# Optimization experiments

Measured on AMD Instinct MI355X. Metric: run time of the kernel, lower is better.

The kernel has to match this reference:

```python
import jax, jax.numpy as jnp
import numpy as np

B, L, E, R, A = 1024, 40, 1024, 1024, 512


def setup_inputs() -> dict:
    key = jax.random.key(0)
    ks = jax.random.split(key, 20)
    s = 0.05  # weight scale to avoid gate saturation
    inp = {
        "xt": jax.random.normal(ks[0], (B, E), jnp.float32),
        "xt_mask": jnp.ones((B, 1), jnp.float32),
        "V": jax.random.normal(ks[1], (B, L, R), jnp.float32),
        "pos_feat": jax.random.normal(ks[2], (B, R), jnp.float32),
        "h1": jax.random.normal(ks[3], (1, B, R), jnp.float32),
        "c1": jax.random.normal(ks[4], (1, B, R), jnp.float32),
        "h2": jax.random.normal(ks[5], (1, B, R), jnp.float32),
        "c2": jax.random.normal(ks[6], (1, B, R), jnp.float32),
        "Wg": jax.random.normal(ks[7], (E, R), jnp.float32) * s,
        "bg": jnp.zeros((R,), jnp.float32),
        "Wi1": jax.random.normal(ks[8], (E, 4 * R), jnp.float32) * s,
        "bi1": jnp.zeros((4 * R,), jnp.float32),
        "Wa1": jax.random.normal(ks[9], (R, 4 * R), jnp.float32) * s,
        "ba1": jnp.zeros((4 * R,), jnp.float32),
        "Wh1": jax.random.normal(ks[10], (R, 4 * R), jnp.float32) * s,
        "bh1": jnp.zeros((4 * R,), jnp.float32),
        "Wi2": jax.random.normal(ks[11], (R, 4 * R), jnp.float32) * s,
        "bi2": jnp.zeros((4 * R,), jnp.float32),
        "Wa2": jax.random.normal(ks[12], (R, 4 * R), jnp.float32) * s,
        "ba2": jnp.zeros((4 * R,), jnp.float32),
        "Wh2": jax.random.normal(ks[13], (R, 4 * R), jnp.float32) * s,
        "bh2": jnp.zeros((4 * R,), jnp.float32),
        "Wv2a": jax.random.normal(ks[14], (R, A), jnp.float32) * s,
        "bv2a": jnp.zeros((A,), jnp.float32),
        "Wh2a": jax.random.normal(ks[15], (2 * R, A), jnp.float32) * s,
        "bh2a": jnp.zeros((A,), jnp.float32),
        "Wa2w": jax.random.normal(ks[16], (A, 1), jnp.float32) * s,
        "ba2w": jnp.zeros((1,), jnp.float32),
    }
    return inp


def _lstm_cell(in1, in2, h, c, Wi, bi, Wa, ba, Wh, bh, mask):
    # all_input_sums: [B, 4R]; torch gate order: i, f, o (sigmoid) then g (tanh)
    s = in1 @ Wi + bi + in2 @ Wa + ba + h @ Wh + bh
    i_g = jax.nn.sigmoid(s[:, 0 * R:1 * R])
    f_g = jax.nn.sigmoid(s[:, 1 * R:2 * R])
    o_g = jax.nn.sigmoid(s[:, 2 * R:3 * R])
    g = jnp.tanh(s[:, 3 * R:4 * R])
    c_new = f_g * c + i_g * g
    c_new = c_new * mask + c * (1.0 - mask)
    h_new = o_g * jnp.tanh(c_new)
    h_new = h_new * mask + h * (1.0 - mask)
    return h_new, c_new


def reference(xt, xt_mask, V, pos_feat, h1, c1, h2, c2,
              Wg, bg, Wi1, bi1, Wa1, ba1, Wh1, bh1,
              Wi2, bi2, Wa2, ba2, Wh2, bh2,
              Wv2a, bv2a, Wh2a, bh2a, Wa2w, ba2w):
    h1l, c1l = h1[-1], c1[-1]  # [B, R]
    h2l, c2l = h2[-1], c2[-1]
    # additive attention over L frames
    hq = jnp.concatenate([h1l, h2l], axis=1) @ Wh2a + bh2a        # [B, A]
    e = jnp.tanh(hq[:, None, :] + V @ Wv2a + bv2a) @ Wa2w + ba2w  # [B, L, 1]
    w = jax.nn.softmax(e, axis=1)                                  # softmax over L
    af = jnp.sum(w * V, axis=1)                                    # [B, R]
    # gate (dropout in eval mode -> identity)
    gate = jax.nn.relu(xt @ Wg + bg)
    gated_pos = gate * pos_feat + pos_feat
    # two-layer LSTM
    out1, c1n = _lstm_cell(xt, gated_pos, h1l, c1l, Wi1, bi1, Wa1, ba1, Wh1, bh1, xt_mask)
    out2, c2n = _lstm_cell(out1, af, h2l, c2l, Wi2, bi2, Wa2, ba2, Wh2, bh2, xt_mask)
    return (out2, out1[None], c1n[None], out2[None], c2n[None])
```

## Files before the change

### kernel.cpp

```cpp
#include <hip/hip_runtime.h>
#include <math.h>

#define BB 1024
#define LL 40
#define RR 1024

using short8 = __attribute__((ext_vector_type(8))) short;
using us8    = __attribute__((ext_vector_type(8))) unsigned short;
using f32x4  = __attribute__((ext_vector_type(4))) float;

__device__ __forceinline__ ushort f2bf(float f) {
    union { float f; unsigned u; } a; a.f = f;
    unsigned r = a.u + 0x7fffu + ((a.u >> 16) & 1u);
    return (ushort)(r >> 16);
}
__device__ __forceinline__ float bf2f(ushort u) {
    union { unsigned u; float f; } a; a.u = ((unsigned)u) << 16;
    return a.f;
}
__device__ __forceinline__ float ftanh(float x) {
    float cx = fminf(fmaxf(x, -15.f), 15.f);
    float e = __expf(2.f * cx);
    return (e - 1.f) / (e + 1.f);
}
__device__ __forceinline__ float fsigmoid(float x) {
    float cx = fminf(fmaxf(x, -30.f), 30.f);
    return 1.f / (1.f + __expf(-cx));
}

__device__ __forceinline__ void gll16(const ushort* g, ushort* l) {
    __builtin_amdgcn_global_load_lds(
        (const __attribute__((address_space(1))) void*)g,
        (__attribute__((address_space(3))) void*)l,
        16, 0, 0);
}

__global__ __launch_bounds__(256) void conv_bf16_kernel(
    const float* __restrict__ src, ushort* __restrict__ dst, int n8)
{
    const int i = blockIdx.x * 256 + threadIdx.x;
    if (i >= n8) return;
    const float4* s4 = (const float4*)(src + (size_t)i * 8);
    float4 x = s4[0], y = s4[1];
    us8 v;
    v[0] = f2bf(x.x); v[1] = f2bf(x.y); v[2] = f2bf(x.z); v[3] = f2bf(x.w);
    v[4] = f2bf(y.x); v[5] = f2bf(y.y); v[6] = f2bf(y.z); v[7] = f2bf(y.w);
    ((us8*)dst)[i] = v;
}

struct CP3 { const float* in[3]; ushort* out[3]; };
__global__ __launch_bounds__(256) void conv_bf16_batch3_kernel(CP3 p, int n8)
{
    const int z = blockIdx.y;
    const int i = blockIdx.x * 256 + threadIdx.x;
    if (i >= n8) return;
    const float4* s4 = (const float4*)(p.in[z] + (size_t)i * 8);
    float4 x = s4[0], y = s4[1];
    us8 v;
    v[0] = f2bf(x.x); v[1] = f2bf(x.y); v[2] = f2bf(x.z); v[3] = f2bf(x.w);
    v[4] = f2bf(y.x); v[5] = f2bf(y.y); v[6] = f2bf(y.z); v[7] = f2bf(y.w);
    ((us8*)p.out[z])[i] = v;
}

struct TP6 { const float* in[6]; ushort* out[6]; int N[6]; };
__global__ __launch_bounds__(256) void transpose_conv_kernel(TP6 p)
{
    const int z = blockIdx.z;
    const int Nn = p.N[z];
    const int n0 = blockIdx.x * 64;
    if (n0 >= Nn) return;
    const int k0 = blockIdx.y * 64;
    const float* in = p.in[z];
    ushort* out = p.out[z];

    __shared__ float tile[64][65];
    const int t = threadIdx.x;
    const int tx = t & 63, ty = t >> 6;
#pragma unroll
    for (int r = 0; r < 16; ++r) {
        const int row = ty * 16 + r;
        tile[row][tx] = in[(size_t)(k0 + row) * Nn + n0 + tx];
    }
    __syncthreads();
    const int n = t >> 2, kq = t & 3;
    us8 v0, v1;
#pragma unroll
    for (int j = 0; j < 8; ++j) v0[j] = f2bf(tile[kq * 16 + j][n]);
#pragma unroll
    for (int j = 0; j < 8; ++j) v1[j] = f2bf(tile[kq * 16 + 8 + j][n]);
    ushort* op = out + (size_t)(n0 + n) * 1024 + k0 + kq * 16;
    *(us8*)op = v0;
    *((us8*)op + 1) = v1;
}

template <int NP, int SK>
__global__ __launch_bounds__(256) void gemm_gl(
    const ushort* __restrict__ A0, const ushort* __restrict__ A1, const ushort* __restrict__ A2,
    const ushort* __restrict__ W0, const ushort* __restrict__ W1, const ushort* __restrict__ W2,
    ushort* __restrict__ Cp, int M, int N)
{
    __shared__ ushort As[128 * 64];
    __shared__ ushort Bs[128 * 64];

    const int t = threadIdx.x, l = t & 63, w = t >> 6;
    const int wm = w >> 1, wn = w & 1;
    const int m0 = blockIdx.y * 128, n0 = blockIdx.x * 128;

    const int srow = l >> 3;
    const int csw  = ((l & 7) ^ (l >> 3)) * 8;
    const int kx0 = ((0 + (l >> 4)) ^ (l & 7)) * 8;
    const int kx1 = ((4 + (l >> 4)) ^ (l & 7)) * 8;

    f32x4 acc[4][4];
#pragma unroll
    for (int i = 0; i < 4; ++i)
#pragma unroll
        for (int j = 0; j < 4; ++j) acc[i][j] = (f32x4){0.f, 0.f, 0.f, 0.f};

    const int total = NP * 16;
    const int per   = total / SK;
    const int s0v   = blockIdx.z * per;
    const int sEnd  = s0v + per;

    for (int s = s0v; s < sEnd; ++s) {
        const int p  = (NP == 1) ? 0 : (s >> 4);
        const int k0 = (s & 15) << 6;
        const ushort* Ap = (p == 0) ? A0 : ((p == 1) ? A1 : A2);
        const ushort* Wp = (p == 0) ? W0 : ((p == 1) ? W1 : W2);
#pragma unroll
        for (int j = 0; j < 4; ++j) {
            const int rb = w * 32 + j * 8;
            gll16(Ap + (size_t)(m0 + rb + srow) * 1024 + k0 + csw, &As[rb * 64]);
            gll16(Wp + (size_t)(n0 + rb + srow) * 1024 + k0 + csw, &Bs[rb * 64]);
        }
        __syncthreads();

        short8 aF[4][2], bF[4][2];
#pragma unroll
        for (int mi = 0; mi < 4; ++mi) {
            const int ro = (wm * 64 + mi * 16 + (l & 15)) * 64;
            aF[mi][0] = *(const short8*)&As[ro + kx0];
            aF[mi][1] = *(const short8*)&As[ro + kx1];
        }
#pragma unroll
        for (int ni = 0; ni < 4; ++ni) {
            const int ro = (wn * 64 + ni * 16 + (l & 15)) * 64;
            bF[ni][0] = *(const short8*)&Bs[ro + kx0];
            bF[ni][1] = *(const short8*)&Bs[ro + kx1];
        }
#pragma unroll
        for (int mi = 0; mi < 4; ++mi)
#pragma unroll
            for (int ni = 0; ni < 4; ++ni) {
                acc[mi][ni] = __builtin_amdgcn_mfma_f32_16x16x32_bf16(
                    aF[mi][0], bF[ni][0], acc[mi][ni], 0, 0, 0);
                acc[mi][ni] = __builtin_amdgcn_mfma_f32_16x16x32_bf16(
                    aF[mi][1], bF[ni][1], acc[mi][ni], 0, 0, 0);
            }
        __syncthreads();
    }

    ushort* Cz = Cp + (size_t)blockIdx.z * M * N;
#pragma unroll
    for (int ni = 0; ni < 4; ++ni) {
        const int col = n0 + wn * 64 + ni * 16 + (l & 15);
#pragma unroll
        for (int mi = 0; mi < 4; ++mi) {
            const int row = m0 + wm * 64 + mi * 16 + ((l >> 4) << 2);
#pragma unroll
            for (int r = 0; r < 4; ++r)
                Cz[(size_t)(row + r) * N + col] = f2bf(acc[mi][ni][r]);
        }
    }
}

__global__ __launch_bounds__(256) void attn_db(
    const ushort* __restrict__ A0, const ushort* __restrict__ W0,
    const float* __restrict__ hq, const float* __restrict__ bv2a,
    const float* __restrict__ Wa2w, float* __restrict__ epart)
{
    __shared__ ushort As[2][128 * 32];
    __shared__ ushort Bs[2][128 * 32];

    const int t = threadIdx.x, l = t & 63, w = t >> 6;
    const int wm = w >> 1, wn = w & 1;

    const int lin = blockIdx.y * gridDim.x + blockIdx.x;
    const int swz = (lin & 7) * 160 + (lin >> 3);
    const int bx = swz & 3, by = swz >> 2;
    const int m0 = by * 128, n0 = bx * 128;

    const int srow  = l >> 2;
    const int schnk = ((l & 3) ^ ((l >> 3) & 3)) * 8;

    int aoff[4], boff[4];
#pragma unroll
    for (int mi = 0; mi < 4; ++mi)
        aoff[mi] = (wm * 64 + mi * 16 + (l & 15)) * 32 + (((l >> 4) ^ ((l >> 1) & 3)) * 8);
#pragma unroll
    for (int ni = 0; ni < 4; ++ni)
        boff[ni] = (wn * 64 + ni * 16 + (l & 15)) * 32 + (((l >> 4) ^ ((l >> 1) & 3)) * 8);

    f32x4 acc[4][4];
#pragma unroll
    for (int i = 0; i < 4; ++i)
#pragma unroll
        for (int j = 0; j < 4; ++j) acc[i][j] = (f32x4){0.f, 0.f, 0.f, 0.f};

    auto stage = [&](int s, int buf) {
        const int k0 = s << 5;
#pragma unroll
        for (int j = 0; j < 2; ++j) {
            const int rb = j * 64 + w * 16;
            gll16(A0 + (size_t)(m0 + rb + srow) * 1024 + k0 + schnk, &As[buf][rb * 32]);
            gll16(W0 + (size_t)(n0 + rb + srow) * 1024 + k0 + schnk, &Bs[buf][rb * 32]);
        }
    };

    constexpr int NS = 32;
    stage(0, 0);
    int cur = 0;
    for (int s = 0; s < NS; ++s) {
        const bool pf = (s + 1 < NS);
        if (pf) {
            stage(s + 1, cur ^ 1);
            asm volatile("s_waitcnt vmcnt(4)" ::: "memory");
        } else {
            asm volatile("s_waitcnt vmcnt(0)" ::: "memory");
        }
        __builtin_amdgcn_s_barrier();
        asm volatile("" ::: "memory");

        short8 aF[4], bF[4];
#pragma unroll
        for (int mi = 0; mi < 4; ++mi) aF[mi] = *(const short8*)&As[cur][aoff[mi]];
#pragma unroll
        for (int ni = 0; ni < 4; ++ni) bF[ni] = *(const short8*)&Bs[cur][boff[ni]];
#pragma unroll
        for (int mi = 0; mi < 4; ++mi)
#pragma unroll
            for (int ni = 0; ni < 4; ++ni)
                acc[mi][ni] = __builtin_amdgcn_mfma_f32_16x16x32_bf16(
                    aF[mi], bF[ni], acc[mi][ni], 0, 0, 0);

        asm volatile("" ::: "memory");
        __builtin_amdgcn_s_barrier();
        asm volatile("" ::: "memory");
        cur ^= 1;
    }

    float* red = (float*)&As[0][0];
    float wa[4], bv[4];
    int coln[4];
#pragma unroll
    for (int ni = 0; ni < 4; ++ni) {
        coln[ni] = n0 + wn * 64 + ni * 16 + (l & 15);
        wa[ni] = Wa2w[coln[ni]];
        bv[ni] = bv2a[coln[ni]];
    }
#pragma unroll
    for (int mi = 0; mi < 4; ++mi) {
        const int rowl = wm * 64 + mi * 16 + ((l >> 4) << 2);
#pragma unroll
        for (int r = 0; r < 4; ++r) {
            const int row = m0 + rowl + r;
            const int b = row / LL;
            float v = 0.f;
#pragma unroll
            for (int ni = 0; ni < 4; ++ni) {
                float x = acc[mi][ni][r] + hq[(size_t)b * 512 + coln[ni]] + bv[ni];
                v += ftanh(x) * wa[ni];
            }
            v += __shfl_xor(v, 1);
            v += __shfl_xor(v, 2);
            v += __shfl_xor(v, 4);
            v += __shfl_xor(v, 8);
            if ((l & 15) == 0) red[(rowl + r) * 2 + wn] = v;
        }
    }
    __syncthreads();
    if (t < 128)
        epart[(size_t)(m0 + t) * 4 + bx] = red[t * 2] + red[t * 2 + 1];
}

__global__ __launch_bounds__(256) void reduce_hq_b_kernel(
    const ushort* __restrict__ part, const float* __restrict__ bias, float* __restrict__ hq)
{
    const int i = blockIdx.x * 256 + threadIdx.x;
    float s = bias[i & 511];
#pragma unroll
    for (int z = 0; z < 8; ++z) s += bf2f(part[(size_t)z * 524288 + i]);
    hq[i] = s;
}

__global__ __launch_bounds__(256) void reduce_gate_b_kernel(
    const ushort* __restrict__ part, const float* __restrict__ bias,
    const float* __restrict__ pos, ushort* __restrict__ gpb)
{
    const int i = blockIdx.x * 256 + threadIdx.x;
    float s = bias[i & 1023];
#pragma unroll
    for (int z = 0; z < 4; ++z) s += bf2f(part[(size_t)z * 1048576 + i]);
    const float g = fmaxf(s, 0.f);
    gpb[i] = f2bf(g * pos[i] + pos[i]);
}

__global__ __launch_bounds__(256) void softmax_af_kernel(
    const float* __restrict__ epart, const ushort* __restrict__ Vb,
    const float* __restrict__ ba2w, ushort* __restrict__ afb)
{
    const int b = blockIdx.x;
    const int tid = threadIdx.x;
    __shared__ float e_raw[LL];
    __shared__ float e_exp[LL];

    if (tid < LL) {
        const float* ep = &epart[(size_t)(b * LL + tid) * 4];
        float e = ba2w[0];
#pragma unroll
        for (int c = 0; c < 4; ++c) e += ep[c];
        e_raw[tid] = e;
    }
    __syncthreads();
    float mx = -1e30f;
#pragma unroll
    for (int ll = 0; ll < LL; ++ll) mx = fmaxf(mx, e_raw[ll]);
    if (tid < LL) e_exp[tid] = __expf(e_raw[tid] - mx);
    __syncthreads();
    float sum = 0.f;
#pragma unroll
    for (int ll = 0; ll < LL; ++ll) sum += e_exp[ll];
    const float inv = 1.f / sum;

    const int r4 = tid * 4;
    const ushort* vp = &Vb[(size_t)b * LL * RR + r4];
    float a0 = 0.f, a1 = 0.f, a2 = 0.f, a3 = 0.f;
#pragma unroll 8
    for (int ll = 0; ll < LL; ++ll) {
        ushort4 v = *(const ushort4*)&vp[(size_t)ll * RR];
        const float wgt = e_exp[ll];
        a0 += wgt * bf2f(v.x); a1 += wgt * bf2f(v.y);
        a2 += wgt * bf2f(v.z); a3 += wgt * bf2f(v.w);
    }
    ushort* op = &afb[(size_t)b * RR + r4];
    op[0] = f2bf(a0 * inv); op[1] = f2bf(a1 * inv);
    op[2] = f2bf(a2 * inv); op[3] = f2bf(a3 * inv);
}

__global__ __launch_bounds__(256) void lstm_finishb_kernel(
    const ushort* __restrict__ part,
    const float* __restrict__ bi, const float* __restrict__ ba, const float* __restrict__ bh,
    const float* __restrict__ c_in, const float* __restrict__ h_in, const float* __restrict__ mask,
    float* __restrict__ h_out, float* __restrict__ h_out2,
    float* __restrict__ c_out, ushort* __restrict__ h_bf)
{
    const int i = blockIdx.x * 256 + threadIdx.x;
    const int b = i >> 10;
    const int r = i & 1023;
    float sg[4];
#pragma unroll
    for (int g = 0; g < 4; ++g) {
        const int gr = g * 1024 + r;
        float s = bi[gr] + ba[gr] + bh[gr];
#pragma unroll
        for (int z = 0; z < 4; ++z)
            s += bf2f(part[(size_t)z * 4194304 + (size_t)b * 4096 + gr]);
        sg[g] = s;
    }
    const float ig = fsigmoid(sg[0]);
    const float fg = fsigmoid(sg[1]);
    const float og = fsigmoid(sg[2]);
    const float gt = ftanh(sg[3]);
    const float m = mask[b];
    const float c = c_in[i];
    float cn = fg * c + ig * gt;
    cn = cn * m + c * (1.f - m);
    const float h = h_in[i];
    float hn = og * ftanh(cn);
    hn = hn * m + h * (1.f - m);
    h_out[i] = hn;
    if (h_out2) h_out2[i] = hn;
    c_out[i] = cn;
    if (h_bf) h_bf[i] = f2bf(hn);
}

extern "C" void kernel_launch(void* const* d_in, const int* in_sizes, int n_in,
                              void* d_out, int out_size, void* d_ws, size_t ws_size,
                              hipStream_t stream) {
    const float* xt   = (const float*)d_in[0];
    const float* mask = (const float*)d_in[1];
    const float* V    = (const float*)d_in[2];
    const float* pos  = (const float*)d_in[3];
    const float* h1   = (const float*)d_in[4];
    const float* c1   = (const float*)d_in[5];
    const float* h2   = (const float*)d_in[6];
    const float* c2   = (const float*)d_in[7];
    const float* Wg   = (const float*)d_in[8];
    const float* bg   = (const float*)d_in[9];
    const float* Wi1  = (const float*)d_in[10];
    const float* bi1  = (const float*)d_in[11];
    const float* Wa1  = (const float*)d_in[12];
    const float* ba1  = (const float*)d_in[13];
    const float* Wh1  = (const float*)d_in[14];
    const float* bh1  = (const float*)d_in[15];
    const float* Wi2  = (const float*)d_in[16];
    const float* bi2  = (const float*)d_in[17];
    const float* Wa2  = (const float*)d_in[18];
    const float* ba2  = (const float*)d_in[19];
    const float* Wh2  = (const float*)d_in[20];
    const float* bh2  = (const float*)d_in[21];
    const float* Wv2a = (const float*)d_in[22];
    const float* bv2a = (const float*)d_in[23];
    const float* Wh2a = (const float*)d_in[24];
    const float* bh2a = (const float*)d_in[25];
    const float* Wa2w = (const float*)d_in[26];
    const float* ba2w = (const float*)d_in[27];

    float* out = (float*)d_out;
    float* out2  = out;
    float* out1  = out + (size_t)BB * RR;
    float* c1n   = out + 2 * (size_t)BB * RR;
    float* out2b = out + 3 * (size_t)BB * RR;
    float* c2n   = out + 4 * (size_t)BB * RR;

    ushort* wsu = (ushort*)d_ws;
    size_t o = 0;
    ushort* Vb     = wsu + o; o += (size_t)40960 * 1024;
    ushort* Wh2aT0 = wsu + o; o += (size_t)512 * 1024;
    ushort* Wh2aT1 = wsu + o; o += (size_t)512 * 1024;
    ushort* WgT    = wsu + o; o += (size_t)1024 * 1024;
    ushort* Wv2aT  = wsu + o; o += (size_t)512 * 1024;
    ushort* Wi1T   = wsu + o; o += (size_t)4096 * 1024;
    ushort* Wa1T   = wsu + o; o += (size_t)4096 * 1024;
    ushort* Wh1T   = wsu + o; o += (size_t)4096 * 1024;
    ushort* Wi2T   = wsu + o; o += (size_t)4096 * 1024;
    ushort* Wa2T   = wsu + o; o += (size_t)4096 * 1024;
    ushort* Wh2T   = wsu + o; o += (size_t)4096 * 1024;
    ushort* xtb    = wsu + o; o += (size_t)1024 * 1024;
    ushort* h1b    = wsu + o; o += (size_t)1024 * 1024;
    ushort* h2b    = wsu + o; o += (size_t)1024 * 1024;
    ushort* gpb    = wsu + o; o += (size_t)1024 * 1024;
    ushort* afb    = wsu + o; o += (size_t)1024 * 1024;
    ushort* out1b  = wsu + o; o += (size_t)1024 * 1024;
    ushort* partSb = wsu + o; o += (size_t)8 * 1024 * 512;
    float* wsf    = (float*)(wsu + o);
    float* hqf    = wsf;
    float* epart  = hqf + 524288;
    ushort* partKb = Vb;

    const dim3 blk(256);

    conv_bf16_kernel<<<dim3(20480), blk, 0, stream>>>(V, Vb, 5242880);
    {
        CP3 p; p.in[0] = xt; p.in[1] = h1; p.in[2] = h2;
        p.out[0] = xtb; p.out[1] = h1b; p.out[2] = h2b;
        conv_bf16_batch3_kernel<<<dim3(512, 3), blk, 0, stream>>>(p, 131072);
    }
    {
        TP6 p;
        p.in[0] = Wi1; p.in[1] = Wa1; p.in[2] = Wh1;
        p.in[3] = Wi2; p.in[4] = Wa2; p.in[5] = Wh2;
        p.out[0] = Wi1T; p.out[1] = Wa1T; p.out[2] = Wh1T;
        p.out[3] = Wi2T; p.out[4] = Wa2T; p.out[5] = Wh2T;
        for (int z = 0; z < 6; ++z) p.N[z] = 4096;
        transpose_conv_kernel<<<dim3(64, 16, 6), blk, 0, stream>>>(p);
    }
    {
        TP6 p;
        p.in[0] = Wh2a; p.in[1] = Wh2a + (size_t)1024 * 512;
        p.in[2] = Wg;   p.in[3] = Wv2a;
        p.out[0] = Wh2aT0; p.out[1] = Wh2aT1; p.out[2] = WgT; p.out[3] = Wv2aT;
        p.N[0] = 512; p.N[1] = 512; p.N[2] = 1024; p.N[3] = 512;
        p.in[4] = nullptr; p.in[5] = nullptr; p.out[4] = nullptr; p.out[5] = nullptr;
        p.N[4] = 0; p.N[5] = 0;
        transpose_conv_kernel<<<dim3(16, 16, 4), blk, 0, stream>>>(p);
    }

    gemm_gl<2, 8><<<dim3(4, 8, 8), blk, 0, stream>>>(
        h1b, h2b, nullptr, Wh2aT0, Wh2aT1, nullptr, partSb, 1024, 512);
    reduce_hq_b_kernel<<<dim3(2048), blk, 0, stream>>>(partSb, bh2a, hqf);

    gemm_gl<1, 4><<<dim3(8, 8, 4), blk, 0, stream>>>(
        xtb, nullptr, nullptr, WgT, nullptr, nullptr, partSb, 1024, 1024);
    reduce_gate_b_kernel<<<dim3(4096), blk, 0, stream>>>(partSb, bg, pos, gpb);

    attn_db<<<dim3(4, 320), blk, 0, stream>>>(
        Vb, Wv2aT, hqf, bv2a, Wa2w, epart);
    softmax_af_kernel<<<dim3(BB), blk, 0, stream>>>(epart, Vb, ba2w, afb);

    gemm_gl<3, 4><<<dim3(32, 8, 4), blk, 0, stream>>>(
        xtb, gpb, h1b, Wi1T, Wa1T, Wh1T, partKb, 1024, 4096);
    lstm_finishb_kernel<<<dim3(4096), blk, 0, stream>>>(
        partKb, bi1, ba1, bh1, c1, h1, mask, out1, nullptr, c1n, out1b);

    gemm_gl<3, 4><<<dim3(32, 8, 4), blk, 0, stream>>>(
        out1b, afb, h2b, Wi2T, Wa2T, Wh2T, partKb, 1024, 4096);
    lstm_finishb_kernel<<<dim3(4096), blk, 0, stream>>>(
        partKb, bi2, ba2, bh2, c2, h2, mask, out2, out2b, c2n, nullptr);
}
```

Before: 312.6 us.

## Widen GEMM tiles to 256x128 and share one templated kernel across stages

Replaces the attention GEMM and the two LSTM gate GEMMs with a templated kernel that uses 256x128 block tiles: 8x4 MFMA accumulators per wave and 2 blocks per CU as the occupancy hint. The larger M tile halves the number of B-tile reloads and doubles arithmetic per loaded byte. The attention epilogue (tanh, dot with Wa2w, row reduce) is kept through a template switch. The cost is higher register pressure and fewer blocks, which reduces parallelism on the 1024-row LSTM GEMMs.

```diff
diff --git a/kernel.cpp b/kernel.cpp
--- a/kernel.cpp
+++ b/kernel.cpp
@@ -174,70 +174,87 @@
     }
 }
 
-__global__ __launch_bounds__(256) void attn_db(
-    const ushort* __restrict__ A0, const ushort* __restrict__ W0,
+template <int NP, int SK, int EPI>
+__global__ __launch_bounds__(256, 2) void gemm_w(
+    const ushort* __restrict__ A0, const ushort* __restrict__ A1, const ushort* __restrict__ A2,
+    const ushort* __restrict__ W0, const ushort* __restrict__ W1, const ushort* __restrict__ W2,
+    ushort* __restrict__ Cp, int M, int N,
     const float* __restrict__ hq, const float* __restrict__ bv2a,
     const float* __restrict__ Wa2w, float* __restrict__ epart)
 {
-    __shared__ ushort As[2][128 * 32];
+    __shared__ ushort As[2][256 * 32];
     __shared__ ushort Bs[2][128 * 32];
 
     const int t = threadIdx.x, l = t & 63, w = t >> 6;
     const int wm = w >> 1, wn = w & 1;
 
-    const int lin = blockIdx.y * gridDim.x + blockIdx.x;
-    const int swz = (lin & 7) * 160 + (lin >> 3);
-    const int bx = swz & 3, by = swz >> 2;
-    const int m0 = by * 128, n0 = bx * 128;
+    int bx, by;
+    if constexpr (EPI == 2) {
+        const int lin = blockIdx.y * gridDim.x + blockIdx.x;
+        const int swz = (lin & 7) * 80 + (lin >> 3);
+        bx = swz & 3; by = swz >> 2;
+    } else { bx = blockIdx.x; by = blockIdx.y; }
+    const int m0 = by * 256, n0 = bx * 128;
 
     const int srow  = l >> 2;
     const int schnk = ((l & 3) ^ ((l >> 3) & 3)) * 8;
 
-    int aoff[4], boff[4];
-#pragma unroll
-    for (int mi = 0; mi < 4; ++mi)
-        aoff[mi] = (wm * 64 + mi * 16 + (l & 15)) * 32 + (((l >> 4) ^ ((l >> 1) & 3)) * 8);
+    int aoff[8], boff[4];
+#pragma unroll
+    for (int mi = 0; mi < 8; ++mi)
+        aoff[mi] = (wm * 128 + mi * 16 + (l & 15)) * 32 + (((l >> 4) ^ ((l >> 1) & 3)) * 8);
 #pragma unroll
     for (int ni = 0; ni < 4; ++ni)
         boff[ni] = (wn * 64 + ni * 16 + (l & 15)) * 32 + (((l >> 4) ^ ((l >> 1) & 3)) * 8);
 
-    f32x4 acc[4][4];
-#pragma unroll
-    for (int i = 0; i < 4; ++i)
+    f32x4 acc[8][4];
+#pragma unroll
+    for (int i = 0; i < 8; ++i)
 #pragma unroll
         for (int j = 0; j < 4; ++j) acc[i][j] = (f32x4){0.f, 0.f, 0.f, 0.f};
 
+    const int total = NP * 32;
+    const int per   = total / SK;
+    const int s0v   = blockIdx.z * per;
+    const int sEnd  = s0v + per;
+
     auto stage = [&](int s, int buf) {
-        const int k0 = s << 5;
+        const int p  = (NP == 1) ? 0 : (s >> 5);
+        const int k0 = (s & 31) << 5;
+        const ushort* Ap = (p == 0) ? A0 : ((p == 1) ? A1 : A2);
+        const ushort* Wp = (p == 0) ? W0 : ((p == 1) ? W1 : W2);
+#pragma unroll
+        for (int j = 0; j < 4; ++j) {
+            const int rb = (w * 4 + j) * 16;
+            gll16(Ap + (size_t)(m0 + rb + srow) * 1024 + k0 + schnk, &As[buf][rb * 32]);
+        }
 #pragma unroll
         for (int j = 0; j < 2; ++j) {
-            const int rb = j * 64 + w * 16;
-            gll16(A0 + (size_t)(m0 + rb + srow) * 1024 + k0 + schnk, &As[buf][rb * 32]);
-            gll16(W0 + (size_t)(n0 + rb + srow) * 1024 + k0 + schnk, &Bs[buf][rb * 32]);
+            const int rb = (w * 2 + j) * 16;
+            gll16(Wp + (size_t)(n0 + rb + srow) * 1024 + k0 + schnk, &Bs[buf][rb * 32]);
         }
     };
 
-    constexpr int NS = 32;
-    stage(0, 0);
+    stage(s0v, 0);
     int cur = 0;
-    for (int s = 0; s < NS; ++s) {
-        const bool pf = (s + 1 < NS);
+    for (int s = s0v; s < sEnd; ++s) {
+        const bool pf = (s + 1 < sEnd);
         if (pf) {
             stage(s + 1, cur ^ 1);
-            asm volatile("s_waitcnt vmcnt(4)" ::: "memory");
+            asm volatile("s_waitcnt vmcnt(6)" ::: "memory");
         } else {
             asm volatile("s_waitcnt vmcnt(0)" ::: "memory");
         }
         __builtin_amdgcn_s_barrier();
         asm volatile("" ::: "memory");
 
-        short8 aF[4], bF[4];
-#pragma unroll
-        for (int mi = 0; mi < 4; ++mi) aF[mi] = *(const short8*)&As[cur][aoff[mi]];
+        short8 aF[8], bF[4];
+#pragma unroll
+        for (int mi = 0; mi < 8; ++mi) aF[mi] = *(const short8*)&As[cur][aoff[mi]];
 #pragma unroll
         for (int ni = 0; ni < 4; ++ni) bF[ni] = *(const short8*)&Bs[cur][boff[ni]];
 #pragma unroll
-        for (int mi = 0; mi < 4; ++mi)
+        for (int mi = 0; mi < 8; ++mi)
 #pragma unroll
             for (int ni = 0; ni < 4; ++ni)
                 acc[mi][ni] = __builtin_amdgcn_mfma_f32_16x16x32_bf16(
@@ -249,38 +266,53 @@
         cur ^= 1;
     }
 
-    float* red = (float*)&As[0][0];
-    float wa[4], bv[4];
-    int coln[4];
-#pragma unroll
-    for (int ni = 0; ni < 4; ++ni) {
-        coln[ni] = n0 + wn * 64 + ni * 16 + (l & 15);
-        wa[ni] = Wa2w[coln[ni]];
-        bv[ni] = bv2a[coln[ni]];
-    }
-#pragma unroll
-    for (int mi = 0; mi < 4; ++mi) {
-        const int rowl = wm * 64 + mi * 16 + ((l >> 4) << 2);
-#pragma unroll
-        for (int r = 0; r < 4; ++r) {
-            const int row = m0 + rowl + r;
-            const int b = row / LL;
-            float v = 0.f;
-#pragma unroll
-            for (int ni = 0; ni < 4; ++ni) {
-                float x = acc[mi][ni][r] + hq[(size_t)b * 512 + coln[ni]] + bv[ni];
-                v += ftanh(x) * wa[ni];
+    if constexpr (EPI == 3) {
+        ushort* Cz = Cp + (size_t)blockIdx.z * M * N;
+#pragma unroll
+        for (int ni = 0; ni < 4; ++ni) {
+            const int col = n0 + wn * 64 + ni * 16 + (l & 15);
+#pragma unroll
+            for (int mi = 0; mi < 8; ++mi) {
+                const int row = m0 + wm * 128 + mi * 16 + ((l >> 4) << 2);
+#pragma unroll
+                for (int r = 0; r < 4; ++r)
+                    Cz[(size_t)(row + r) * N + col] = f2bf(acc[mi][ni][r]);
             }
-            v += __shfl_xor(v, 1);
-            v += __shfl_xor(v, 2);
-            v += __shfl_xor(v, 4);
-            v += __shfl_xor(v, 8);
-            if ((l & 15) == 0) red[(rowl + r) * 2 + wn] = v;
-        }
-    }
-    __syncthreads();
-    if (t < 128)
-        epart[(size_t)(m0 + t) * 4 + bx] = red[t * 2] + red[t * 2 + 1];
+        }
+    } else if constexpr (EPI == 2) {
+        float* red = (float*)&As[0][0];
+        float wa[4], bv[4];
+        int coln[4];
+#pragma unroll
+        for (int ni = 0; ni < 4; ++ni) {
+            coln[ni] = n0 + wn * 64 + ni * 16 + (l & 15);
+            wa[ni] = Wa2w[coln[ni]];
+            bv[ni] = bv2a[coln[ni]];
+        }
+#pragma unroll
+        for (int mi = 0; mi < 8; ++mi) {
+            const int rowl = wm * 128 + mi * 16 + ((l >> 4) << 2);
+#pragma unroll
+            for (int r = 0; r < 4; ++r) {
+                const int row = m0 + rowl + r;
+                const int b = row / LL;
+                float v = 0.f;
+#pragma unroll
+                for (int ni = 0; ni < 4; ++ni) {
+                    float x = acc[mi][ni][r] + hq[(size_t)b * 512 + coln[ni]] + bv[ni];
+                    v += ftanh(x) * wa[ni];
+                }
+                v += __shfl_xor(v, 1);
+                v += __shfl_xor(v, 2);
+                v += __shfl_xor(v, 4);
+                v += __shfl_xor(v, 8);
+                if ((l & 15) == 0) red[(rowl + r) * 2 + wn] = v;
+            }
+        }
+        __syncthreads();
+        if (t < 256)
+            epart[(size_t)(m0 + t) * 4 + bx] = red[t * 2] + red[t * 2 + 1];
+    }
 }
 
 __global__ __launch_bounds__(256) void reduce_hq_b_kernel(
@@ -484,17 +516,20 @@
         xtb, nullptr, nullptr, WgT, nullptr, nullptr, partSb, 1024, 1024);
     reduce_gate_b_kernel<<<dim3(4096), blk, 0, stream>>>(partSb, bg, pos, gpb);
 
-    attn_db<<<dim3(4, 320), blk, 0, stream>>>(
-        Vb, Wv2aT, hqf, bv2a, Wa2w, epart);
+    gemm_w<1, 1, 2><<<dim3(4, 160), blk, 0, stream>>>(
+        Vb, nullptr, nullptr, Wv2aT, nullptr, nullptr,
+        nullptr, 40960, 512, hqf, bv2a, Wa2w, epart);
     softmax_af_kernel<<<dim3(BB), blk, 0, stream>>>(epart, Vb, ba2w, afb);
 
-    gemm_gl<3, 4><<<dim3(32, 8, 4), blk, 0, stream>>>(
-        xtb, gpb, h1b, Wi1T, Wa1T, Wh1T, partKb, 1024, 4096);
+    gemm_w<3, 4, 3><<<dim3(32, 4, 4), blk, 0, stream>>>(
+        xtb, gpb, h1b, Wi1T, Wa1T, Wh1T,
+        partKb, 1024, 4096, nullptr, nullptr, nullptr, nullptr);
     lstm_finishb_kernel<<<dim3(4096), blk, 0, stream>>>(
         partKb, bi1, ba1, bh1, c1, h1, mask, out1, nullptr, c1n, out1b);
 
-    gemm_gl<3, 4><<<dim3(32, 8, 4), blk, 0, stream>>>(
-        out1b, afb, h2b, Wi2T, Wa2T, Wh2T, partKb, 1024, 4096);
+    gemm_w<3, 4, 3><<<dim3(32, 4, 4), blk, 0, stream>>>(
+        out1b, afb, h2b, Wi2T, Wa2T, Wh2T,
+        partKb, 1024, 4096, nullptr, nullptr, nullptr, nullptr);
     lstm_finishb_kernel<<<dim3(4096), blk, 0, stream>>>(
         partKb, bi2, ba2, bh2, c2, h2, mask, out2, out2b, c2n, nullptr);
 }
```

New measurement: 410.8 us. 1.31x slower.
